# Optimization experiments

Measured on AMD Instinct MI355X. Metric: run time of the kernel, lower is better.

The kernel has to match this reference:

```python
import jax, jax.numpy as jnp
import numpy as np

N_NODES = 50000
N_EDGES = 20000
EDGE_SIZE = 32
IN_CH = 256
OUT_CH = 256


def setup_inputs() -> dict:
    key = jax.random.key(0)
    k1, k2, k3 = jax.random.split(key, 3)
    x = jax.random.normal(k1, (N_NODES, IN_CH), dtype=jnp.float32)
    hyperedges = jax.random.randint(k2, (N_EDGES, EDGE_SIZE), 0, N_NODES)
    weight = jax.random.normal(k3, (IN_CH, OUT_CH), dtype=jnp.float32)
    return {"x": x, "hyperedges": hyperedges, "weight": weight}


def reference(x, hyperedges, weight):
    # Gather node features per hyperedge and reduce ('sum' aggregation):
    # [E, K, C] -> [E, C]
    edge_sum = x[hyperedges].sum(axis=1)
    # Scatter-add each hyperedge's summed feature back to every member node.
    agg = jnp.zeros_like(x).at[hyperedges].add(edge_sum[:, None, :])
    # Dense projection + ReLU.
    return jax.nn.relu(agg @ weight)
```

## Files before the change

kernel.cpp:

```cpp
#include <hip/hip_runtime.h>
#include <hip/hip_bf16.h>

#define N_NODES 50000
#define N_EDGES 20000
#define EDGE_K  32
#define CH      256
#define N_INC   (N_EDGES * EDGE_K)
#define ELL_CAP 64
#define NSLICE  8
#define SCH     32

typedef __attribute__((ext_vector_type(4))) float f32x4;
typedef __attribute__((ext_vector_type(8))) short bf16x8;

static __device__ __forceinline__ unsigned short f2bf(float f) {
    __hip_bfloat16 h = __float2bfloat16(f);
    return *reinterpret_cast<unsigned short*>(&h);
}
static __device__ __forceinline__ float bflo(unsigned int u) {
    unsigned int b = u << 16;
    float f; __builtin_memcpy(&f, &b, 4); return f;
}
static __device__ __forceinline__ float bfhi(unsigned int u) {
    unsigned int b = u & 0xffff0000u;
    float f; __builtin_memcpy(&f, &b, 4); return f;
}
static __device__ __forceinline__ unsigned int pk2(float a, float b) {
    return (unsigned int)f2bf(a) | ((unsigned int)f2bf(b) << 16);
}

#define CONV_BLOCKS (N_NODES * CH / 8 / 256)
#define ZERO_BLOCKS ((N_NODES + 255) / 256)
__global__ void prep_kernel(const float* __restrict__ x, unsigned short* __restrict__ xb,
                            const float* __restrict__ w, unsigned short* __restrict__ wt,
                            int* __restrict__ deg) {
    int b = blockIdx.x;
    if (b < CONV_BLOCKS) {
        int i = b * 256 + threadIdx.x;
        int n = i >> 5, sub = i & 31;
        int g = sub >> 2, cp = (sub & 3) * 8;
        const float* src = x + (size_t)n * CH + sub * 8;
        f32x4 v0 = *reinterpret_cast<const f32x4*>(src);
        f32x4 v1 = *reinterpret_cast<const f32x4*>(src + 4);
        uint4 u;
        u.x = pk2(v0.x, v0.y);
        u.y = pk2(v0.z, v0.w);
        u.z = pk2(v1.x, v1.y);
        u.w = pk2(v1.z, v1.w);
        *reinterpret_cast<uint4*>(xb + ((size_t)g * N_NODES + n) * SCH + cp) = u;
    } else if (b < CONV_BLOCKS + CH) {
        int n = b - CONV_BLOCKS;
        int k = threadIdx.x;
        wt[n * CH + k] = f2bf(w[k * CH + n]);
    } else {
        int i = (b - CONV_BLOCKS - CH) * 256 + threadIdx.x;
        if (i < N_NODES) deg[i] = 0;
    }
}

#define FILL_GROUPS   8
#define NODES_PER_GRP (N_NODES / FILL_GROUPS)
#define FILL_WIN      2560
#define FILL_BLOCKS   ((N_INC / FILL_WIN) * FILL_GROUPS)
#define GGRP          (N_EDGES / 16)
#define GATHER_BLOCKS (GGRP * NSLICE)
__global__ __launch_bounds__(256) void gather_fill_kernel(
        const unsigned short* __restrict__ xb, const int* __restrict__ he,
        unsigned short* __restrict__ es, int* __restrict__ deg,
        unsigned short* __restrict__ ell) {
    int b = blockIdx.x;
    if (b < FILL_BLOCKS) {
        int g  = b % FILL_GROUPS;
        int wn = b / FILL_GROUPS;
        int lo = g * NODES_PER_GRP, hi = lo + NODES_PER_GRP;
        int base = wn * FILL_WIN;
#pragma unroll
        for (int it = 0; it < FILL_WIN / 256; ++it) {
            int i = base + it * 256 + threadIdx.x;
            int node = he[i];
            if (node >= lo && node < hi) {
                int slot = atomicAdd(&deg[node], 1);
                if (slot < ELL_CAP)
                    ell[(size_t)node * ELL_CAP + slot] = (unsigned short)(i >> 5);
            }
        }
        return;
    }
    int gb  = b - FILL_BLOCKS;
    int g   = gb & 7;
    int grp = gb >> 3;
    int w = threadIdx.x >> 6, lane = threadIdx.x & 63;
    int ebase = grp * 16 + w * 4;
    const int* hp = he + (size_t)ebase * EDGE_K;
    int s = lane & 15;
    int ep = lane >> 4, k = (lane >> 2) & 3, q = lane & 3;
    int mA = hp[ep * 32 + s];
    int mB = hp[ep * 32 + 16 + s];
    const unsigned short* xg = xb + (size_t)g * N_NODES * SCH;
    float a[8] = {0.f, 0.f, 0.f, 0.f, 0.f, 0.f, 0.f, 0.f};
#pragma unroll
    for (int r = 0; r < 8; ++r) {
        int e = __shfl((r < 4) ? mA : mB, (lane & 48) + ((r * 4 + k) & 15), 64);
        uint4 d = *reinterpret_cast<const uint4*>(xg + (size_t)e * SCH + q * 8);
        a[0] += bflo(d.x); a[1] += bfhi(d.x);
        a[2] += bflo(d.y); a[3] += bfhi(d.y);
        a[4] += bflo(d.z); a[5] += bfhi(d.z);
        a[6] += bflo(d.w); a[7] += bfhi(d.w);
    }
#pragma unroll
    for (int j = 0; j < 8; ++j) a[j] += __shfl_xor(a[j], 4, 64);
#pragma unroll
    for (int j = 0; j < 8; ++j) a[j] += __shfl_xor(a[j], 8, 64);
    if ((lane & 12) == 0) {
        uint4 u;
        u.x = pk2(a[0], a[1]);
        u.y = pk2(a[2], a[3]);
        u.z = pk2(a[4], a[5]);
        u.w = pk2(a[6], a[7]);
        *reinterpret_cast<uint4*>(es + (size_t)(ebase + ep) * CH + g * SCH + q * 8) = u;
    }
}

__global__ __launch_bounds__(256) void gemm_kernel(const unsigned short* __restrict__ es,
                                                   const unsigned short* __restrict__ wt,
                                                   unsigned short* __restrict__ yb) {
    int wid  = threadIdx.x >> 6;
    int lane = threadIdx.x & 63;
    int m0   = blockIdx.x * 64 + wid * 16;
    if (m0 >= N_EDGES) return;
    int lr = lane & 15;
    int lg = lane >> 4;

    f32x4 acc[16] = {};
    const unsigned short* arow = es + (size_t)(m0 + lr) * CH + lg * 8;
#pragma unroll
    for (int kk = 0; kk < CH; kk += 32) {
        bf16x8 a = *reinterpret_cast<const bf16x8*>(arow + kk);
#pragma unroll
        for (int nt = 0; nt < 16; ++nt) {
            bf16x8 bb = *reinterpret_cast<const bf16x8*>(
                wt + (size_t)(nt * 16 + lr) * CH + kk + lg * 8);
            acc[nt] = __builtin_amdgcn_mfma_f32_16x16x32_bf16(a, bb, acc[nt], 0, 0, 0);
        }
    }
#pragma unroll
    for (int nt = 0; nt < 16; ++nt) {
#pragma unroll
        for (int r = 0; r < 4; ++r) {
            int row = m0 + lg * 4 + r;
            yb[((size_t)(nt >> 1) * N_EDGES + row) * SCH + (nt & 1) * 16 + lr] =
                f2bf(acc[nt][r]);
        }
    }
}

#define AP_NPB    16
#define AP_BLOCKS ((N_NODES / AP_NPB) * NSLICE)
__global__ __launch_bounds__(256) void apply_kernel(
        const unsigned short* __restrict__ yb, const int* __restrict__ deg,
        const unsigned short* __restrict__ ell, float* __restrict__ out) {
    int b = blockIdx.x;
    int g = b & 7;
    int w = threadIdx.x >> 6, lane = threadIdx.x & 63;
    int np = lane >> 4, s = lane & 15, k = (lane >> 2) & 3, q = lane & 3;
    int node = (b >> 3) * AP_NPB + w * 4 + np;
    int d = deg[node];
    if (d > ELL_CAP) d = ELL_CAP;
    const unsigned short* er = ell + (size_t)node * ELL_CAP;
    int m0 = er[s], m1 = er[16 + s], m2 = er[32 + s], m3 = er[48 + s];
    int dmax = d;
    dmax = max(dmax, __shfl_xor(dmax, 16, 64));
    dmax = max(dmax, __shfl_xor(dmax, 32, 64));
    const unsigned short* yg = yb + (size_t)g * N_EDGES * SCH;
    float a[8] = {0.f, 0.f, 0.f, 0.f, 0.f, 0.f, 0.f, 0.f};
#pragma unroll
    for (int rq = 0; rq < 4; ++rq) {
        if (rq * 16 >= dmax) break;
        int m = (rq == 0) ? m0 : (rq == 1) ? m1 : (rq == 2) ? m2 : m3;
#pragma unroll
        for (int rr = 0; rr < 4; ++rr) {
            int slot = rq * 16 + rr * 4 + k;
            int e = __shfl(m, (lane & 48) + rr * 4 + k, 64);
            if (slot < d) {
                uint4 dd = *reinterpret_cast<const uint4*>(yg + (size_t)e * SCH + q * 8);
                a[0] += bflo(dd.x); a[1] += bfhi(dd.x);
                a[2] += bflo(dd.y); a[3] += bfhi(dd.y);
                a[4] += bflo(dd.z); a[5] += bfhi(dd.z);
                a[6] += bflo(dd.w); a[7] += bfhi(dd.w);
            }
        }
    }
#pragma unroll
    for (int j = 0; j < 8; ++j) a[j] += __shfl_xor(a[j], 4, 64);
#pragma unroll
    for (int j = 0; j < 8; ++j) a[j] += __shfl_xor(a[j], 8, 64);
    if ((lane & 12) == 0) {
        f32x4 r0, r1;
        r0.x = fmaxf(a[0], 0.f); r0.y = fmaxf(a[1], 0.f);
        r0.z = fmaxf(a[2], 0.f); r0.w = fmaxf(a[3], 0.f);
        r1.x = fmaxf(a[4], 0.f); r1.y = fmaxf(a[5], 0.f);
        r1.z = fmaxf(a[6], 0.f); r1.w = fmaxf(a[7], 0.f);
        float* dst = out + (size_t)node * CH + g * SCH + q * 8;
        *reinterpret_cast<f32x4*>(dst)     = r0;
        *reinterpret_cast<f32x4*>(dst + 4) = r1;
    }
}

extern "C" void kernel_launch(void* const* d_in, const int* in_sizes, int n_in,
                              void* d_out, int out_size, void* d_ws, size_t ws_size,
                              hipStream_t stream) {
    const float* x  = (const float*)d_in[0];
    const int*   he = (const int*)d_in[1];
    const float* w  = (const float*)d_in[2];
    float* out = (float*)d_out;

    char* ws = (char*)d_ws;
    unsigned short* wt  = (unsigned short*)ws;
    unsigned short* es  = (unsigned short*)(ws + 131072);
    unsigned short* yb  = (unsigned short*)(ws + 131072 + 10240000);
    int* deg = (int*)(ws + 131072 + 10240000 + 10240000);
    unsigned short* ell = (unsigned short*)(ws + 131072 + 10240000 + 10240000 + 200000);

    unsigned short* xb = (unsigned short*)d_out;

    prep_kernel<<<CONV_BLOCKS + CH + ZERO_BLOCKS, 256, 0, stream>>>(x, xb, w, wt, deg);

    gather_fill_kernel<<<FILL_BLOCKS + GATHER_BLOCKS, 256, 0, stream>>>(xb, he, es, deg, ell);

    {
        int blocks = (N_EDGES + 63) / 64;
        gemm_kernel<<<blocks, 256, 0, stream>>>(es, wt, yb);
    }

    apply_kernel<<<AP_BLOCKS, 256, 0, stream>>>(yb, deg, ell, out);
}
```

Measured before the change: 145.4 us.

## Switch intermediates to fp16 with packed half2 sums and zero-row ELL padding

Stores x, the weight matrix, the edge sums and the projected edge features as fp16 instead of bf16. Gathers and reductions now accumulate with packed __hadd2 instead of unpacking to fp32, and the GEMM uses the f16 MFMA. ELL slots are pre-filled with a sentinel index pointing at an added zero row of yb, so the apply loop drops its per-slot degree check. Gather loads are issued up front, and the gather kernel gets a launch-bounds occupancy hint. The aim is fewer ALU and conversion instructions and less branching in the gather phases, at the cost of fp16 accumulation precision and range risk plus an extra prep pass that initialises the ELL table.

```diff
diff --git a/kernel.cpp b/kernel.cpp
--- a/kernel.cpp
+++ b/kernel.cpp
@@ -1,5 +1,6 @@
 #include <hip/hip_runtime.h>
 #include <hip/hip_bf16.h>
+#include <hip/hip_fp16.h>
 
 #define N_NODES 50000
 #define N_EDGES 20000
@@ -9,31 +10,28 @@
 #define ELL_CAP 64
 #define NSLICE  8
 #define SCH     32
+#define ZROW    N_EDGES
 
 typedef __attribute__((ext_vector_type(4))) float f32x4;
-typedef __attribute__((ext_vector_type(8))) short bf16x8;
-
-static __device__ __forceinline__ unsigned short f2bf(float f) {
-    __hip_bfloat16 h = __float2bfloat16(f);
-    return *reinterpret_cast<unsigned short*>(&h);
-}
-static __device__ __forceinline__ float bflo(unsigned int u) {
-    unsigned int b = u << 16;
-    float f; __builtin_memcpy(&f, &b, 4); return f;
-}
-static __device__ __forceinline__ float bfhi(unsigned int u) {
-    unsigned int b = u & 0xffff0000u;
-    float f; __builtin_memcpy(&f, &b, 4); return f;
-}
-static __device__ __forceinline__ unsigned int pk2(float a, float b) {
-    return (unsigned int)f2bf(a) | ((unsigned int)f2bf(b) << 16);
+typedef __attribute__((ext_vector_type(8))) _Float16 f16x8;
+
+static __device__ __forceinline__ __half2 u2h2(unsigned int u) {
+    __half2 h; __builtin_memcpy(&h, &u, 4); return h;
+}
+static __device__ __forceinline__ unsigned int h22u(__half2 h) {
+    unsigned int u; __builtin_memcpy(&u, &h, 4); return u;
+}
+static __device__ __forceinline__ unsigned int pk2h(float a, float b) {
+    return h22u(__halves2half2(__float2half_rn(a), __float2half_rn(b)));
 }
 
 #define CONV_BLOCKS (N_NODES * CH / 8 / 256)
 #define ZERO_BLOCKS ((N_NODES + 255) / 256)
+#define ELLI_BLOCKS (N_NODES * ELL_CAP / 2 / 256)
 __global__ void prep_kernel(const float* __restrict__ x, unsigned short* __restrict__ xb,
                             const float* __restrict__ w, unsigned short* __restrict__ wt,
-                            int* __restrict__ deg) {
+                            int* __restrict__ deg, unsigned int* __restrict__ ellu,
+                            unsigned short* __restrict__ yb) {
     int b = blockIdx.x;
     if (b < CONV_BLOCKS) {
         int i = b * 256 + threadIdx.x;
@@ -43,18 +41,25 @@
         f32x4 v0 = *reinterpret_cast<const f32x4*>(src);
         f32x4 v1 = *reinterpret_cast<const f32x4*>(src + 4);
         uint4 u;
-        u.x = pk2(v0.x, v0.y);
-        u.y = pk2(v0.z, v0.w);
-        u.z = pk2(v1.x, v1.y);
-        u.w = pk2(v1.z, v1.w);
+        u.x = pk2h(v0.x, v0.y);
+        u.y = pk2h(v0.z, v0.w);
+        u.z = pk2h(v1.x, v1.y);
+        u.w = pk2h(v1.z, v1.w);
         *reinterpret_cast<uint4*>(xb + ((size_t)g * N_NODES + n) * SCH + cp) = u;
     } else if (b < CONV_BLOCKS + CH) {
         int n = b - CONV_BLOCKS;
         int k = threadIdx.x;
-        wt[n * CH + k] = f2bf(w[k * CH + n]);
-    } else {
+        __half h = __float2half_rn(w[k * CH + n]);
+        wt[n * CH + k] = *reinterpret_cast<unsigned short*>(&h);
+    } else if (b < CONV_BLOCKS + CH + ZERO_BLOCKS) {
         int i = (b - CONV_BLOCKS - CH) * 256 + threadIdx.x;
         if (i < N_NODES) deg[i] = 0;
+    } else if (b < CONV_BLOCKS + CH + ZERO_BLOCKS + ELLI_BLOCKS) {
+        int i = (b - CONV_BLOCKS - CH - ZERO_BLOCKS) * 256 + threadIdx.x;
+        ellu[i] = 0x4E204E20u;
+    } else {
+        int g = threadIdx.x >> 5, c = threadIdx.x & 31;
+        yb[((size_t)g * (N_EDGES + 1) + ZROW) * SCH + c] = 0;
     }
 }
 
@@ -64,7 +69,7 @@
 #define FILL_BLOCKS   ((N_INC / FILL_WIN) * FILL_GROUPS)
 #define GGRP          (N_EDGES / 16)
 #define GATHER_BLOCKS (GGRP * NSLICE)
-__global__ __launch_bounds__(256) void gather_fill_kernel(
+__global__ __launch_bounds__(256, 4) void gather_fill_kernel(
         const unsigned short* __restrict__ xb, const int* __restrict__ he,
         unsigned short* __restrict__ es, int* __restrict__ deg,
         unsigned short* __restrict__ ell) {
@@ -97,26 +102,51 @@
     int mA = hp[ep * 32 + s];
     int mB = hp[ep * 32 + 16 + s];
     const unsigned short* xg = xb + (size_t)g * N_NODES * SCH;
-    float a[8] = {0.f, 0.f, 0.f, 0.f, 0.f, 0.f, 0.f, 0.f};
-#pragma unroll
-    for (int r = 0; r < 8; ++r) {
-        int e = __shfl((r < 4) ? mA : mB, (lane & 48) + ((r * 4 + k) & 15), 64);
-        uint4 d = *reinterpret_cast<const uint4*>(xg + (size_t)e * SCH + q * 8);
-        a[0] += bflo(d.x); a[1] += bfhi(d.x);
-        a[2] += bflo(d.y); a[3] += bfhi(d.y);
-        a[4] += bflo(d.z); a[5] += bfhi(d.z);
-        a[6] += bflo(d.w); a[7] += bfhi(d.w);
-    }
-#pragma unroll
-    for (int j = 0; j < 8; ++j) a[j] += __shfl_xor(a[j], 4, 64);
-#pragma unroll
-    for (int j = 0; j < 8; ++j) a[j] += __shfl_xor(a[j], 8, 64);
+    int hb = lane & 48;
+    int e0 = __shfl(mA, hb + ((0 + k) & 15), 64);
+    int e1 = __shfl(mA, hb + ((4 + k) & 15), 64);
+    int e2 = __shfl(mA, hb + ((8 + k) & 15), 64);
+    int e3 = __shfl(mA, hb + ((12 + k) & 15), 64);
+    int e4 = __shfl(mB, hb + ((0 + k) & 15), 64);
+    int e5 = __shfl(mB, hb + ((4 + k) & 15), 64);
+    int e6 = __shfl(mB, hb + ((8 + k) & 15), 64);
+    int e7 = __shfl(mB, hb + ((12 + k) & 15), 64);
+    uint4 d0 = *reinterpret_cast<const uint4*>(xg + (size_t)e0 * SCH + q * 8);
+    uint4 d1 = *reinterpret_cast<const uint4*>(xg + (size_t)e1 * SCH + q * 8);
+    uint4 d2 = *reinterpret_cast<const uint4*>(xg + (size_t)e2 * SCH + q * 8);
+    uint4 d3 = *reinterpret_cast<const uint4*>(xg + (size_t)e3 * SCH + q * 8);
+    uint4 d4 = *reinterpret_cast<const uint4*>(xg + (size_t)e4 * SCH + q * 8);
+    uint4 d5 = *reinterpret_cast<const uint4*>(xg + (size_t)e5 * SCH + q * 8);
+    uint4 d6 = *reinterpret_cast<const uint4*>(xg + (size_t)e6 * SCH + q * 8);
+    uint4 d7 = *reinterpret_cast<const uint4*>(xg + (size_t)e7 * SCH + q * 8);
+    __half2 a0 = u2h2(0u), a1 = u2h2(0u), a2 = u2h2(0u), a3 = u2h2(0u);
+    a0 = __hadd2(a0, u2h2(d0.x)); a1 = __hadd2(a1, u2h2(d0.y));
+    a2 = __hadd2(a2, u2h2(d0.z)); a3 = __hadd2(a3, u2h2(d0.w));
+    a0 = __hadd2(a0, u2h2(d1.x)); a1 = __hadd2(a1, u2h2(d1.y));
+    a2 = __hadd2(a2, u2h2(d1.z)); a3 = __hadd2(a3, u2h2(d1.w));
+    a0 = __hadd2(a0, u2h2(d2.x)); a1 = __hadd2(a1, u2h2(d2.y));
+    a2 = __hadd2(a2, u2h2(d2.z)); a3 = __hadd2(a3, u2h2(d2.w));
+    a0 = __hadd2(a0, u2h2(d3.x)); a1 = __hadd2(a1, u2h2(d3.y));
+    a2 = __hadd2(a2, u2h2(d3.z)); a3 = __hadd2(a3, u2h2(d3.w));
+    a0 = __hadd2(a0, u2h2(d4.x)); a1 = __hadd2(a1, u2h2(d4.y));
+    a2 = __hadd2(a2, u2h2(d4.z)); a3 = __hadd2(a3, u2h2(d4.w));
+    a0 = __hadd2(a0, u2h2(d5.x)); a1 = __hadd2(a1, u2h2(d5.y));
+    a2 = __hadd2(a2, u2h2(d5.z)); a3 = __hadd2(a3, u2h2(d5.w));
+    a0 = __hadd2(a0, u2h2(d6.x)); a1 = __hadd2(a1, u2h2(d6.y));
+    a2 = __hadd2(a2, u2h2(d6.z)); a3 = __hadd2(a3, u2h2(d6.w));
+    a0 = __hadd2(a0, u2h2(d7.x)); a1 = __hadd2(a1, u2h2(d7.y));
+    a2 = __hadd2(a2, u2h2(d7.z)); a3 = __hadd2(a3, u2h2(d7.w));
+    a0 = __hadd2(a0, u2h2(__shfl_xor(h22u(a0), 4, 64)));
+    a1 = __hadd2(a1, u2h2(__shfl_xor(h22u(a1), 4, 64)));
+    a2 = __hadd2(a2, u2h2(__shfl_xor(h22u(a2), 4, 64)));
+    a3 = __hadd2(a3, u2h2(__shfl_xor(h22u(a3), 4, 64)));
+    a0 = __hadd2(a0, u2h2(__shfl_xor(h22u(a0), 8, 64)));
+    a1 = __hadd2(a1, u2h2(__shfl_xor(h22u(a1), 8, 64)));
+    a2 = __hadd2(a2, u2h2(__shfl_xor(h22u(a2), 8, 64)));
+    a3 = __hadd2(a3, u2h2(__shfl_xor(h22u(a3), 8, 64)));
     if ((lane & 12) == 0) {
         uint4 u;
-        u.x = pk2(a[0], a[1]);
-        u.y = pk2(a[2], a[3]);
-        u.z = pk2(a[4], a[5]);
-        u.w = pk2(a[6], a[7]);
+        u.x = h22u(a0); u.y = h22u(a1); u.z = h22u(a2); u.w = h22u(a3);
         *reinterpret_cast<uint4*>(es + (size_t)(ebase + ep) * CH + g * SCH + q * 8) = u;
     }
 }
@@ -135,12 +165,12 @@
     const unsigned short* arow = es + (size_t)(m0 + lr) * CH + lg * 8;
 #pragma unroll
     for (int kk = 0; kk < CH; kk += 32) {
-        bf16x8 a = *reinterpret_cast<const bf16x8*>(arow + kk);
+        f16x8 a = *reinterpret_cast<const f16x8*>(arow + kk);
 #pragma unroll
         for (int nt = 0; nt < 16; ++nt) {
-            bf16x8 bb = *reinterpret_cast<const bf16x8*>(
+            f16x8 bb = *reinterpret_cast<const f16x8*>(
                 wt + (size_t)(nt * 16 + lr) * CH + kk + lg * 8);
-            acc[nt] = __builtin_amdgcn_mfma_f32_16x16x32_bf16(a, bb, acc[nt], 0, 0, 0);
+            acc[nt] = __builtin_amdgcn_mfma_f32_16x16x32_f16(a, bb, acc[nt], 0, 0, 0);
         }
     }
 #pragma unroll
@@ -148,8 +178,9 @@
 #pragma unroll
         for (int r = 0; r < 4; ++r) {
             int row = m0 + lg * 4 + r;
-            yb[((size_t)(nt >> 1) * N_EDGES + row) * SCH + (nt & 1) * 16 + lr] =
-                f2bf(acc[nt][r]);
+            __half h = __float2half_rn(acc[nt][r]);
+            yb[((size_t)(nt >> 1) * (N_EDGES + 1) + row) * SCH + (nt & 1) * 16 + lr] =
+                *reinterpret_cast<unsigned short*>(&h);
         }
     }
 }
@@ -171,35 +202,47 @@
     int dmax = d;
     dmax = max(dmax, __shfl_xor(dmax, 16, 64));
     dmax = max(dmax, __shfl_xor(dmax, 32, 64));
-    const unsigned short* yg = yb + (size_t)g * N_EDGES * SCH;
-    float a[8] = {0.f, 0.f, 0.f, 0.f, 0.f, 0.f, 0.f, 0.f};
-#pragma unroll
+    const unsigned short* yg = yb + (size_t)g * (N_EDGES + 1) * SCH;
+    int hb = lane & 48;
+    __half2 a0 = u2h2(0u), a1 = u2h2(0u), a2 = u2h2(0u), a3 = u2h2(0u);
     for (int rq = 0; rq < 4; ++rq) {
         if (rq * 16 >= dmax) break;
         int m = (rq == 0) ? m0 : (rq == 1) ? m1 : (rq == 2) ? m2 : m3;
-#pragma unroll
-        for (int rr = 0; rr < 4; ++rr) {
-            int slot = rq * 16 + rr * 4 + k;
-            int e = __shfl(m, (lane & 48) + rr * 4 + k, 64);
-            if (slot < d) {
-                uint4 dd = *reinterpret_cast<const uint4*>(yg + (size_t)e * SCH + q * 8);
-                a[0] += bflo(dd.x); a[1] += bfhi(dd.x);
-                a[2] += bflo(dd.y); a[3] += bfhi(dd.y);
-                a[4] += bflo(dd.z); a[5] += bfhi(dd.z);
-                a[6] += bflo(dd.w); a[7] += bfhi(dd.w);
-            }
-        }
-    }
-#pragma unroll
-    for (int j = 0; j < 8; ++j) a[j] += __shfl_xor(a[j], 4, 64);
-#pragma unroll
-    for (int j = 0; j < 8; ++j) a[j] += __shfl_xor(a[j], 8, 64);
+        int e0 = __shfl(m, hb + 0 + k, 64);
+        int e1 = __shfl(m, hb + 4 + k, 64);
+        int e2 = __shfl(m, hb + 8 + k, 64);
+        int e3 = __shfl(m, hb + 12 + k, 64);
+        uint4 d0 = *reinterpret_cast<const uint4*>(yg + (size_t)e0 * SCH + q * 8);
+        uint4 d1 = *reinterpret_cast<const uint4*>(yg + (size_t)e1 * SCH + q * 8);
+        uint4 d2 = *reinterpret_cast<const uint4*>(yg + (size_t)e2 * SCH + q * 8);
+        uint4 d3 = *reinterpret_cast<const uint4*>(yg + (size_t)e3 * SCH + q * 8);
+        a0 = __hadd2(a0, u2h2(d0.x)); a1 = __hadd2(a1, u2h2(d0.y));
+        a2 = __hadd2(a2, u2h2(d0.z)); a3 = __hadd2(a3, u2h2(d0.w));
+        a0 = __hadd2(a0, u2h2(d1.x)); a1 = __hadd2(a1, u2h2(d1.y));
+        a2 = __hadd2(a2, u2h2(d1.z)); a3 = __hadd2(a3, u2h2(d1.w));
+        a0 = __hadd2(a0, u2h2(d2.x)); a1 = __hadd2(a1, u2h2(d2.y));
+        a2 = __hadd2(a2, u2h2(d2.z)); a3 = __hadd2(a3, u2h2(d2.w));
+        a0 = __hadd2(a0, u2h2(d3.x)); a1 = __hadd2(a1, u2h2(d3.y));
+        a2 = __hadd2(a2, u2h2(d3.z)); a3 = __hadd2(a3, u2h2(d3.w));
+    }
+    a0 = __hadd2(a0, u2h2(__shfl_xor(h22u(a0), 4, 64)));
+    a1 = __hadd2(a1, u2h2(__shfl_xor(h22u(a1), 4, 64)));
+    a2 = __hadd2(a2, u2h2(__shfl_xor(h22u(a2), 4, 64)));
+    a3 = __hadd2(a3, u2h2(__shfl_xor(h22u(a3), 4, 64)));
+    a0 = __hadd2(a0, u2h2(__shfl_xor(h22u(a0), 8, 64)));
+    a1 = __hadd2(a1, u2h2(__shfl_xor(h22u(a1), 8, 64)));
+    a2 = __hadd2(a2, u2h2(__shfl_xor(h22u(a2), 8, 64)));
+    a3 = __hadd2(a3, u2h2(__shfl_xor(h22u(a3), 8, 64)));
     if ((lane & 12) == 0) {
+        float2 f0 = __half22float2(a0);
+        float2 f1 = __half22float2(a1);
+        float2 f2 = __half22float2(a2);
+        float2 f3 = __half22float2(a3);
         f32x4 r0, r1;
-        r0.x = fmaxf(a[0], 0.f); r0.y = fmaxf(a[1], 0.f);
-        r0.z = fmaxf(a[2], 0.f); r0.w = fmaxf(a[3], 0.f);
-        r1.x = fmaxf(a[4], 0.f); r1.y = fmaxf(a[5], 0.f);
-        r1.z = fmaxf(a[6], 0.f); r1.w = fmaxf(a[7], 0.f);
+        r0.x = fmaxf(f0.x, 0.f); r0.y = fmaxf(f0.y, 0.f);
+        r0.z = fmaxf(f1.x, 0.f); r0.w = fmaxf(f1.y, 0.f);
+        r1.x = fmaxf(f2.x, 0.f); r1.y = fmaxf(f2.y, 0.f);
+        r1.z = fmaxf(f3.x, 0.f); r1.w = fmaxf(f3.y, 0.f);
         float* dst = out + (size_t)node * CH + g * SCH + q * 8;
         *reinterpret_cast<f32x4*>(dst)     = r0;
         *reinterpret_cast<f32x4*>(dst + 4) = r1;
@@ -217,13 +260,14 @@
     char* ws = (char*)d_ws;
     unsigned short* wt  = (unsigned short*)ws;
     unsigned short* es  = (unsigned short*)(ws + 131072);
-    unsigned short* yb  = (unsigned short*)(ws + 131072 + 10240000);
-    int* deg = (int*)(ws + 131072 + 10240000 + 10240000);
-    unsigned short* ell = (unsigned short*)(ws + 131072 + 10240000 + 10240000 + 200000);
+    unsigned short* yb  = (unsigned short*)(ws + 10371072);
+    int* deg = (int*)(ws + 20611584);
+    unsigned short* ell = (unsigned short*)(ws + 20811584);
 
     unsigned short* xb = (unsigned short*)d_out;
 
-    prep_kernel<<<CONV_BLOCKS + CH + ZERO_BLOCKS, 256, 0, stream>>>(x, xb, w, wt, deg);
+    prep_kernel<<<CONV_BLOCKS + CH + ZERO_BLOCKS + ELLI_BLOCKS + 1, 256, 0, stream>>>(
+        x, xb, w, wt, deg, (unsigned int*)ell, yb);
 
     gather_fill_kernel<<<FILL_BLOCKS + GATHER_BLOCKS, 256, 0, stream>>>(xb, he, es, deg, ell);
 
```

New measurement: 140.9 us, median of 2. -3.1%, faster.
